# Kernel optimization log

Measured on AMD Instinct MI355X. Metric: run time of the kernel, lower is better.

## Reference

```python
import jax, jax.numpy as jnp
import numpy as np
from jax import lax

NORM = 8.0  # SFA_neuron Norm and Quant max_value
NUM_HEADS = 8

@jax.custom_vjp
def quant(u):
    return jnp.round(jnp.clip(u, 0.0, NORM))

def _quant_fwd(u):
    return quant(u), u

def _quant_bwd(u, g):
    # straight-through: zero grad where input outside [0, NORM]
    return (jnp.where((u >= 0.0) & (u <= NORM), g, 0.0),)

quant.defvjp(_quant_fwd, _quant_bwd)

def sfa(x):
    # x: [T, ...]; recurrent membrane state h carried across timesteps
    def step(h, xt):
        u = h + xt
        s = quant(u)
        return u - s, s / NORM
    _, y = lax.scan(step, jnp.zeros_like(x[0]), x)
    return y

def conv_bn(x, w, scale, bias):
    # 1x1 conv (no bias) + BatchNorm2d (inference, folded to affine)
    # x: [T,B,Cin,H,W], w: [Cout,Cin]
    y = jnp.einsum('oc,tbchw->tbohw', w, x)
    return y * scale[None, None, :, None, None] + bias[None, None, :, None, None]

def setup_inputs() -> dict:
    key = jax.random.key(0)
    ks = jax.random.split(key, 13)
    T, B, C, H, W = 4, 32, 512, 16, 16
    Cv = 4 * C  # lamda_ratio = 4
    f32 = jnp.float32
    d = {}
    d['x'] = jax.random.normal(ks[0], (T, B, C, H, W), f32)
    d['wq'] = jax.random.normal(ks[1], (C, C), f32) * (1.0 / np.sqrt(C))
    d['wk'] = jax.random.normal(ks[2], (C, C), f32) * (1.0 / np.sqrt(C))
    d['wv'] = jax.random.normal(ks[3], (Cv, C), f32) * (1.0 / np.sqrt(C))
    d['wp'] = jax.random.normal(ks[4], (C, Cv), f32) * (1.0 / np.sqrt(Cv))
    d['q_scale'] = 1.0 + 0.1 * jax.random.normal(ks[5], (C,), f32)
    d['q_bias'] = 0.1 * jax.random.normal(ks[6], (C,), f32)
    d['k_scale'] = 1.0 + 0.1 * jax.random.normal(ks[7], (C,), f32)
    d['k_bias'] = 0.1 * jax.random.normal(ks[8], (C,), f32)
    d['v_scale'] = 1.0 + 0.1 * jax.random.normal(ks[9], (Cv,), f32)
    d['v_bias'] = 0.1 * jax.random.normal(ks[10], (Cv,), f32)
    d['p_scale'] = 1.0 + 0.1 * jax.random.normal(ks[11], (C,), f32)
    d['p_bias'] = 0.1 * jax.random.normal(ks[12], (C,), f32)
    return d

def _to_heads(t, h):
    # [T,B,C,H,W] -> [T,B,h,N,C//h]  (channel c -> head c//dh, feat c%dh)
    T_, B_, C_, H_, W_ = t.shape
    return t.reshape(T_, B_, h, C_ // h, H_ * W_).transpose(0, 1, 2, 4, 3)

def reference(x, wq, wk, wv, wp, q_scale, q_bias, k_scale, k_bias, v_scale, v_bias, p_scale, p_bias):
    T, B, C, H, W = x.shape
    N = H * W
    Cv = wv.shape[0]
    scale = (C // NUM_HEADS) ** -0.5

    xs = sfa(x)  # head_spike
    q = sfa(conv_bn(xs, wq, q_scale, q_bias))
    k = sfa(conv_bn(xs, wk, k_scale, k_bias))
    v = sfa(conv_bn(xs, wv, v_scale, v_bias))

    qh = _to_heads(q, NUM_HEADS)  # [T,B,h,N,dh]
    kh = _to_heads(k, NUM_HEADS)
    vh = _to_heads(v, NUM_HEADS)  # [T,B,h,N,dv]

    attn = jnp.einsum('tbhnd,tbhmd->tbhnm', qh, kh)          # [T,B,h,N,N]
    out = jnp.einsum('tbhnm,tbhme->tbhne', attn, vh) * (scale * 2.0)

    out = out.transpose(0, 1, 2, 4, 3).reshape(T, B, Cv, N)  # [T,B,Cv,N]
    out = sfa(out)                                            # attn_spike
    out = out.reshape(T, B, Cv, H, W)
    out = conv_bn(out, wp, p_scale, p_bias)                   # [T,B,C,H,W]
    return out
```

## Files before the change

### kernel.cpp

```cpp
#include <hip/hip_runtime.h>
#include <hip/hip_bf16.h>

#define T_  4
#define B_  32
#define C_  512
#define CV_ 2048
#define N_  256
#define NH_ 8
#define DH_ 64
#define DV_ 256

typedef __bf16 bf16_t;
typedef __bf16 bf16x8 __attribute__((ext_vector_type(8)));
typedef float  f32x4  __attribute__((ext_vector_type(4)));
typedef unsigned char u8x8 __attribute__((ext_vector_type(8)));

#if defined(__has_builtin)
# if __has_builtin(__builtin_amdgcn_global_load_lds)
#  define USE_GLL 1
# endif
#endif

__device__ __forceinline__ f32x4 mfma16(bf16x8 a, bf16x8 b, f32x4 c) {
  return __builtin_amdgcn_mfma_f32_16x16x32_bf16(a, b, c, 0, 0, 0);
}

__device__ __forceinline__ float quant_step(float u) {
  return rintf(fminf(fmaxf(u, 0.0f), 8.0f));
}

__device__ __forceinline__ bf16x8 cvt8(u8x8 v) {
  bf16x8 r;
#pragma unroll
  for (int j = 0; j < 8; ++j) r[j] = (bf16_t)(float)(unsigned int)v[j];
  return r;
}

__device__ __forceinline__ void stage16(const void* g, void* lbase, int lane) {
#ifdef USE_GLL
  __builtin_amdgcn_global_load_lds(
      (const __attribute__((address_space(1))) void*)g,
      (__attribute__((address_space(3))) void*)lbase, 16, 0, 0);
#else
  *(uint4*)((char*)lbase + lane * 16) = *(const uint4*)g;
#endif
}

__global__ __launch_bounds__(256) void k0_split(const float* __restrict__ src,
                                                bf16_t* __restrict__ hi,
                                                bf16_t* __restrict__ lo, int n8) {
  int i = blockIdx.x * 256 + threadIdx.x;
  if (i >= n8) return;
  const float* s = src + (size_t)i * 8;
  bf16x8 h, l;
#pragma unroll
  for (int j = 0; j < 8; ++j) {
    float w = s[j];
    __bf16 hh = (__bf16)w;
    h[j] = hh;
    l[j] = (__bf16)(w - (float)hh);
  }
  *(bf16x8*)(hi + (size_t)i * 8) = h;
  *(bf16x8*)(lo + (size_t)i * 8) = l;
}

__global__ __launch_bounds__(256) void k1_sfa_x(const float* __restrict__ x,
                                                unsigned char* __restrict__ xsT) {
  __shared__ unsigned char tile[64 * 80];
  int bt = blockIdx.x;
  int b  = blockIdx.y;
  int tid = threadIdx.x;
  int c0 = (bt >> 2) * 64, n0 = (bt & 3) * 64;
  int cl = tid >> 2, nc = (tid & 3) * 16;
  int nl = tid >> 2, cj = (tid & 3) * 16;

  float h[16];
#pragma unroll
  for (int j = 0; j < 16; ++j) h[j] = 0.0f;

  for (int t = 0; t < T_; ++t) {
    const float* xp = x + ((size_t)(t * B_ + b) * C_ + c0 + cl) * N_ + n0 + nc;
    f32x4 xv[4];
#pragma unroll
    for (int j = 0; j < 4; ++j) xv[j] = *(const f32x4*)(xp + j * 4);
    if (t) __syncthreads();
#pragma unroll
    for (int j = 0; j < 16; ++j) {
      float u = __fadd_rn(h[j], xv[j >> 2][j & 3]);
      float s = quant_step(u);
      h[j] = __fsub_rn(u, s);
      tile[(nc + j) * 80 + cl] = (unsigned char)s;
    }
    __syncthreads();
    uint4 o = *(const uint4*)&tile[nl * 80 + cj];
    *(uint4*)(xsT + ((size_t)(t * B_ + b) * N_ + n0 + nl) * C_ + c0 + cj) = o;
  }
}

template<bool SWAPQ>
__global__ __launch_bounds__(256, 3) void k2_qkv(
    const unsigned char* __restrict__ xsT,
    const bf16_t* __restrict__ w_hi, const bf16_t* __restrict__ w_lo,
    const float* __restrict__ q_scale, const float* __restrict__ q_bias,
    const float* __restrict__ k_scale, const float* __restrict__ k_bias,
    const float* __restrict__ v_scale, const float* __restrict__ v_bias,
    unsigned char* __restrict__ q_s8, unsigned char* __restrict__ k_s8,
    unsigned char* __restrict__ v_s8, int ct_off) {
  __shared__ __align__(16) unsigned char xs_l[T_][4][1024];
  __shared__ __align__(16) bf16_t whi_l[64 * 64];
  __shared__ __align__(16) bf16_t wlo_l[64 * 64];

  int ct = blockIdx.x + ct_off;
  int ntile = blockIdx.y, b = blockIdx.z;
  int tid = threadIdx.x;
  int w = tid >> 6, lane = tid & 63, quad = lane >> 4, l16 = lane & 15;

  int mode, co_out;
  const float *scp, *bip;
  if (ct < 8)       { mode = 0; co_out = ct * 64;        scp = q_scale; bip = q_bias; }
  else if (ct < 16) { mode = 1; co_out = (ct - 8) * 64;  scp = k_scale; bip = k_bias; }
  else              { mode = 2; co_out = (ct - 16) * 64; scp = v_scale; bip = v_bias; }

  const bf16_t* wrow = w_hi + (size_t)ct * 64 * C_;
  const bf16_t* lrow = w_lo + (size_t)ct * 64 * C_;
  int n0b = ntile * 64;

  int r4 = lane >> 2, m4 = lane & 3;
  int sw4 = (r4 + (r4 >> 2)) & 3;
  int r8 = lane >> 3, m8 = lane & 7;

  f32x4 acc[T_][4];
#pragma unroll
  for (int t = 0; t < T_; ++t)
#pragma unroll
    for (int mt = 0; mt < 4; ++mt) acc[t][mt] = (f32x4){0.f, 0.f, 0.f, 0.f};

  for (int kc = 0; kc < 8; ++kc) {
    int c0 = kc * 64;
    __syncthreads();
#pragma unroll
    for (int t = 0; t < T_; ++t) {
      const unsigned char* g = xsT +
          ((size_t)(t * B_ + b) * N_ + n0b + w * 16 + r4) * C_ + c0 + ((m4 ^ sw4) << 4);
      stage16(g, &xs_l[t][w][0], lane);
    }
#pragma unroll
    for (int j = 0; j < 2; ++j) {
      int r0 = w * 16 + j * 8;
      int row = r0 + r8;
      int col = c0 + ((m8 ^ (row & 7)) << 3);
      stage16(wrow + (size_t)row * C_ + col, (char*)whi_l + r0 * 128, lane);
      stage16(lrow + (size_t)row * C_ + col, (char*)wlo_l + r0 * 128, lane);
    }
    __syncthreads();
#pragma unroll
    for (int ks = 0; ks < 2; ++ks) {
      int kb = ks * 4 + quad;
      int slot = (kb >> 1) ^ ((l16 + (l16 >> 2)) & 3);
      int xoff = l16 * 64 + slot * 16 + (kb & 1) * 8;
      bf16x8 bx[T_];
#pragma unroll
      for (int t = 0; t < T_; ++t)
        bx[t] = cvt8(*(const u8x8*)((const char*)&xs_l[t][w][0] + xoff));
#pragma unroll
      for (int mt = 0; mt < 4; ++mt) {
        int row = mt * 16 + l16;
        int woff = row * 128 + ((kb ^ (row & 7)) << 4);
        bf16x8 ah = *(const bf16x8*)((const char*)whi_l + woff);
        bf16x8 al = *(const bf16x8*)((const char*)wlo_l + woff);
#pragma unroll
        for (int t = 0; t < T_; ++t) {
          if (SWAPQ) {
            acc[t][mt] = mfma16(bx[t], ah, acc[t][mt]);
            acc[t][mt] = mfma16(bx[t], al, acc[t][mt]);
          } else {
            acc[t][mt] = mfma16(ah, bx[t], acc[t][mt]);
            acc[t][mt] = mfma16(al, bx[t], acc[t][mt]);
          }
        }
      }
    }
  }
  if (SWAPQ) {
    float sc[4], bi[4], h[4][4];
#pragma unroll
    for (int mt = 0; mt < 4; ++mt) {
      int c = co_out + mt * 16 + l16;
      sc[mt] = __fmul_rn(q_scale[c], 0.125f);
      bi[mt] = q_bias[c];
#pragma unroll
      for (int r = 0; r < 4; ++r) h[mt][r] = 0.0f;
    }
#pragma unroll
    for (int t = 0; t < T_; ++t)
#pragma unroll
      for (int mt = 0; mt < 4; ++mt)
#pragma unroll
        for (int r = 0; r < 4; ++r) {
          float y = __fmul_rn(acc[t][mt][r], sc[mt]);
          y = __fadd_rn(y, bi[mt]);
          float u = __fadd_rn(h[mt][r], y);
          float s = quant_step(u);
          h[mt][r] = __fsub_rn(u, s);
          int n = n0b + w * 16 + quad * 4 + r;
          int c = co_out + mt * 16 + l16;
          q_s8[((size_t)(t * B_ + b) * N_ + n) * C_ + c] = (unsigned char)s;
        }
  } else {
    float sc[4][4], bi[4][4], h[4][4];
#pragma unroll
    for (int mt = 0; mt < 4; ++mt)
#pragma unroll
      for (int r = 0; r < 4; ++r) {
        int c = co_out + mt * 16 + quad * 4 + r;
        sc[mt][r] = __fmul_rn(scp[c], 0.125f);
        bi[mt][r] = bip[c];
        h[mt][r] = 0.0f;
      }
#pragma unroll
    for (int t = 0; t < T_; ++t)
#pragma unroll
      for (int mt = 0; mt < 4; ++mt)
#pragma unroll
        for (int r = 0; r < 4; ++r) {
          float y = __fmul_rn(acc[t][mt][r], sc[mt][r]);
          y = __fadd_rn(y, bi[mt][r]);
          float u = __fadd_rn(h[mt][r], y);
          float s = quant_step(u);
          h[mt][r] = __fsub_rn(u, s);
          int n = n0b + w * 16 + l16;
          int c = co_out + mt * 16 + quad * 4 + r;
          unsigned char sp = (unsigned char)s;
          if (mode == 1) k_s8[((size_t)(t * B_ + b) * C_ + c) * N_ + n] = sp;
          else           v_s8[((size_t)(t * B_ + b) * CV_ + c) * N_ + n] = sp;
        }
  }
}

__global__ __launch_bounds__(256) void k3_attn(
    const unsigned char* __restrict__ q_s8, const unsigned char* __restrict__ k_s8,
    const unsigned char* __restrict__ v_s8, unsigned char* __restrict__ a_s8) {
  __shared__ float kvbuf[64 * 68];
  int et = blockIdx.x, hh = blockIdx.y, b = blockIdx.z;
  int tid = threadIdx.x;
  int w = tid >> 6, lane = tid & 63, quad = lane >> 4, l16 = lane & 15;
  int e0 = et * 64;

  f32x4 Aacc[4][4];
#pragma unroll
  for (int mt = 0; mt < 4; ++mt)
#pragma unroll
    for (int nt = 0; nt < 4; ++nt) Aacc[mt][nt] = (f32x4){0.f, 0.f, 0.f, 0.f};

  for (int t = 0; t < T_; ++t) {
    size_t tb = (size_t)(t * B_ + b);
    f32x4 kva[4];
#pragma unroll
    for (int et2 = 0; et2 < 4; ++et2) kva[et2] = (f32x4){0.f, 0.f, 0.f, 0.f};
    const unsigned char* krow  = k_s8 + ((size_t)tb * C_ + hh * DH_ + w * 16 + l16) * N_;
    const unsigned char* vbase = v_s8 + ((size_t)tb * CV_ + hh * DV_ + e0) * N_;
    for (int kc = 0; kc < 8; ++kc) {
      int koff = kc * 32 + quad * 8;
      bf16x8 a = cvt8(*(const u8x8*)(krow + koff));
#pragma unroll
      for (int et2 = 0; et2 < 4; ++et2) {
        bf16x8 bb = cvt8(*(const u8x8*)(vbase + (size_t)(et2 * 16 + l16) * N_ + koff));
        kva[et2] = mfma16(a, bb, kva[et2]);
      }
    }
    __syncthreads();
#pragma unroll
    for (int et2 = 0; et2 < 4; ++et2)
#pragma unroll
      for (int r = 0; r < 4; ++r)
        kvbuf[(w * 16 + quad * 4 + r) * 68 + et2 * 16 + l16] = kva[et2][r];
    __syncthreads();

    const unsigned char* qrow = q_s8 + ((size_t)tb * N_ + w * 64) * C_ + hh * DH_;
    for (int kc2 = 0; kc2 < 2; ++kc2) {
      int kbase = kc2 * 32 + quad * 8;
      bf16x8 bq[4];
#pragma unroll
      for (int nt = 0; nt < 4; ++nt)
        bq[nt] = cvt8(*(const u8x8*)(qrow + (size_t)(nt * 16 + l16) * C_ + kbase));
#pragma unroll
      for (int mt = 0; mt < 4; ++mt) {
        bf16x8 ahi, alo;
#pragma unroll
        for (int j = 0; j < 8; ++j) {
          float v = kvbuf[(kbase + j) * 68 + mt * 16 + l16] * 0.015625f;
          __bf16 hi = (__bf16)v;
          ahi[j] = hi;
          alo[j] = (__bf16)(v - (float)hi);
        }
#pragma unroll
        for (int nt = 0; nt < 4; ++nt) {
          Aacc[mt][nt] = mfma16(ahi, bq[nt], Aacc[mt][nt]);
          Aacc[mt][nt] = mfma16(alo, bq[nt], Aacc[mt][nt]);
        }
      }
    }
#pragma unroll
    for (int mt = 0; mt < 4; ++mt)
#pragma unroll
      for (int nt = 0; nt < 4; ++nt)
#pragma unroll
        for (int r = 0; r < 4; ++r) {
          float u = Aacc[mt][nt][r] * 0.03125f;
          float s = quant_step(u);
          int cv = hh * DV_ + e0 + mt * 16 + quad * 4 + r;
          int n  = w * 64 + nt * 16 + l16;
          a_s8[(tb * N_ + n) * CV_ + cv] = (unsigned char)s;
          Aacc[mt][nt][r] = __fsub_rn(Aacc[mt][nt][r], 32.0f * s);
        }
  }
}

__global__ __launch_bounds__(256, 3) void k4_pconv(
    const unsigned char* __restrict__ a_s8,
    const bf16_t* __restrict__ wp_hi, const bf16_t* __restrict__ wp_lo,
    const float* __restrict__ p_scale, const float* __restrict__ p_bias,
    float* __restrict__ out) {
  __shared__ __align__(16) unsigned char as_l[4][4][1024];
  __shared__ __align__(16) bf16_t whi_l[64 * 64];
  __shared__ __align__(16) bf16_t wlo_l[64 * 64];

  int ct = blockIdx.x, ntile = blockIdx.y, tbq = blockIdx.z;
  int tid = threadIdx.x;
  int w = tid >> 6, lane = tid & 63, quad = lane >> 4, l16 = lane & 15;
  int co0 = ct * 64, n0b = ntile * 64;

  int r4 = lane >> 2, m4 = lane & 3;
  int sw4 = (r4 + (r4 >> 2)) & 3;
  int r8 = lane >> 3, m8 = lane & 7;

  const bf16_t* wrow = wp_hi + (size_t)co0 * CV_;
  const bf16_t* lrow = wp_lo + (size_t)co0 * CV_;

  f32x4 acc[4][4];
#pragma unroll
  for (int i = 0; i < 4; ++i)
#pragma unroll
    for (int mt = 0; mt < 4; ++mt) acc[i][mt] = (f32x4){0.f, 0.f, 0.f, 0.f};

  for (int kc = 0; kc < 32; ++kc) {
    int c0 = kc * 64;
    __syncthreads();
#pragma unroll
    for (int tbi = 0; tbi < 4; ++tbi) {
      const unsigned char* g = a_s8 +
          ((size_t)(tbq * 4 + tbi) * N_ + n0b + w * 16 + r4) * CV_ + c0 + ((m4 ^ sw4) << 4);
      stage16(g, &as_l[tbi][w][0], lane);
    }
#pragma unroll
    for (int j = 0; j < 2; ++j) {
      int r0 = w * 16 + j * 8;
      int row = r0 + r8;
      int col = c0 + ((m8 ^ (row & 7)) << 3);
      stage16(wrow + (size_t)row * CV_ + col, (char*)whi_l + r0 * 128, lane);
      stage16(lrow + (size_t)row * CV_ + col, (char*)wlo_l + r0 * 128, lane);
    }
    __syncthreads();
#pragma unroll
    for (int ks = 0; ks < 2; ++ks) {
      int kb = ks * 4 + quad;
      int slot = (kb >> 1) ^ ((l16 + (l16 >> 2)) & 3);
      int xoff = l16 * 64 + slot * 16 + (kb & 1) * 8;
      bf16x8 bx[4];
#pragma unroll
      for (int tbi = 0; tbi < 4; ++tbi)
        bx[tbi] = cvt8(*(const u8x8*)((const char*)&as_l[tbi][w][0] + xoff));
#pragma unroll
      for (int mt = 0; mt < 4; ++mt) {
        int row = mt * 16 + l16;
        int woff = row * 128 + ((kb ^ (row & 7)) << 4);
        bf16x8 ah = *(const bf16x8*)((const char*)whi_l + woff);
        bf16x8 al = *(const bf16x8*)((const char*)wlo_l + woff);
#pragma unroll
        for (int tbi = 0; tbi < 4; ++tbi) {
          acc[tbi][mt] = mfma16(ah, bx[tbi], acc[tbi][mt]);
          acc[tbi][mt] = mfma16(al, bx[tbi], acc[tbi][mt]);
        }
      }
    }
  }
#pragma unroll
  for (int mt = 0; mt < 4; ++mt)
#pragma unroll
    for (int r = 0; r < 4; ++r) {
      int c = co0 + mt * 16 + quad * 4 + r;
      float scv = __fmul_rn(p_scale[c], 0.125f);
      float biv = p_bias[c];
#pragma unroll
      for (int tbi = 0; tbi < 4; ++tbi) {
        float y = __fmul_rn(acc[tbi][mt][r], scv);
        y = __fadd_rn(y, biv);
        int n = n0b + w * 16 + l16;
        out[((size_t)(tbq * 4 + tbi) * C_ + c) * N_ + n] = y;
      }
    }
}

extern "C" void kernel_launch(void* const* d_in, const int* in_sizes, int n_in,
                              void* d_out, int out_size, void* d_ws, size_t ws_size,
                              hipStream_t stream) {
  const float* x       = (const float*)d_in[0];
  const float* wq      = (const float*)d_in[1];
  const float* wk      = (const float*)d_in[2];
  const float* wv      = (const float*)d_in[3];
  const float* wp      = (const float*)d_in[4];
  const float* q_scale = (const float*)d_in[5];
  const float* q_bias  = (const float*)d_in[6];
  const float* k_scale = (const float*)d_in[7];
  const float* k_bias  = (const float*)d_in[8];
  const float* v_scale = (const float*)d_in[9];
  const float* v_bias  = (const float*)d_in[10];
  const float* p_scale = (const float*)d_in[11];
  const float* p_bias  = (const float*)d_in[12];

  const size_t MB = 1024 * 1024;
  if (ws_size < 160 * MB) return;
  char* ws = (char*)d_ws;
  unsigned char* xsT    = (unsigned char*)(ws);
  unsigned char* a_s8   = (unsigned char*)(ws);
  bf16_t*        wqkv_h = (bf16_t*)(ws + 32 * MB);
  bf16_t*        wqkv_l = (bf16_t*)(ws + 35 * MB);
  unsigned char* q_s8   = (unsigned char*)(ws + 64 * MB);
  bf16_t*        wp_h   = (bf16_t*)(ws + 64 * MB);
  bf16_t*        wp_l   = (bf16_t*)(ws + 66 * MB);
  unsigned char* k_s8   = (unsigned char*)(ws + 80 * MB);
  unsigned char* v_s8   = (unsigned char*)(ws + 96 * MB);

  k0_split<<<128, 256, 0, stream>>>(wq, wqkv_h, wqkv_l, 32768);
  k0_split<<<128, 256, 0, stream>>>(wk, wqkv_h + 262144, wqkv_l + 262144, 32768);
  k0_split<<<512, 256, 0, stream>>>(wv, wqkv_h + 524288, wqkv_l + 524288, 131072);

  k1_sfa_x<<<dim3(32, B_), 256, 0, stream>>>(x, xsT);
  k2_qkv<true><<<dim3(8, 4, B_), 256, 0, stream>>>(
      xsT, wqkv_h, wqkv_l, q_scale, q_bias, k_scale, k_bias,
      v_scale, v_bias, q_s8, k_s8, v_s8, 0);
  k2_qkv<false><<<dim3(40, 4, B_), 256, 0, stream>>>(
      xsT, wqkv_h, wqkv_l, q_scale, q_bias, k_scale, k_bias,
      v_scale, v_bias, q_s8, k_s8, v_s8, 8);
  k3_attn<<<dim3(4, NH_, B_), 256, 0, stream>>>(q_s8, k_s8, v_s8, a_s8);
  k0_split<<<512, 256, 0, stream>>>(wp, wp_h, wp_l, 131072);
  k4_pconv<<<dim3(8, 4, B_), 256, 0, stream>>>(a_s8, wp_h, wp_l,
                                               p_scale, p_bias, (float*)d_out);
}
```

Baseline: 586.5 us.

## Double-buffer LDS staging in QKV and projection conv kernels

Converts the k2_qkv and k4_pconv main loops to a double-buffered LDS pipeline. The next K-chunk is prefetched into the alternate buffer while the current one is consumed by MFMAs, and one barrier per iteration replaces two. s_setprio is raised around the MFMA section. The larger shared-memory footprint comes with a launch_bounds occupancy hint lowered from 3 to 2 blocks per CU, trading occupancy for latency hiding.

```diff
diff --git a/kernel.cpp b/kernel.cpp
--- a/kernel.cpp
+++ b/kernel.cpp
@@ -98,7 +98,7 @@
 }
 
 template<bool SWAPQ>
-__global__ __launch_bounds__(256, 3) void k2_qkv(
+__global__ __launch_bounds__(256, 2) void k2_qkv(
     const unsigned char* __restrict__ xsT,
     const bf16_t* __restrict__ w_hi, const bf16_t* __restrict__ w_lo,
     const float* __restrict__ q_scale, const float* __restrict__ q_bias,
@@ -106,9 +106,9 @@
     const float* __restrict__ v_scale, const float* __restrict__ v_bias,
     unsigned char* __restrict__ q_s8, unsigned char* __restrict__ k_s8,
     unsigned char* __restrict__ v_s8, int ct_off) {
-  __shared__ __align__(16) unsigned char xs_l[T_][4][1024];
-  __shared__ __align__(16) bf16_t whi_l[64 * 64];
-  __shared__ __align__(16) bf16_t wlo_l[64 * 64];
+  __shared__ __align__(16) unsigned char xs_l[2][T_][4][1024];
+  __shared__ __align__(16) bf16_t whi_l[2][64 * 64];
+  __shared__ __align__(16) bf16_t wlo_l[2][64 * 64];
 
   int ct = blockIdx.x + ct_off;
   int ntile = blockIdx.y, b = blockIdx.z;
@@ -135,24 +135,31 @@
 #pragma unroll
     for (int mt = 0; mt < 4; ++mt) acc[t][mt] = (f32x4){0.f, 0.f, 0.f, 0.f};
 
-  for (int kc = 0; kc < 8; ++kc) {
+  auto STAGE = [&](int kc, int pb) {
     int c0 = kc * 64;
-    __syncthreads();
 #pragma unroll
     for (int t = 0; t < T_; ++t) {
       const unsigned char* g = xsT +
           ((size_t)(t * B_ + b) * N_ + n0b + w * 16 + r4) * C_ + c0 + ((m4 ^ sw4) << 4);
-      stage16(g, &xs_l[t][w][0], lane);
+      stage16(g, &xs_l[pb][t][w][0], lane);
     }
 #pragma unroll
     for (int j = 0; j < 2; ++j) {
       int r0 = w * 16 + j * 8;
       int row = r0 + r8;
       int col = c0 + ((m8 ^ (row & 7)) << 3);
-      stage16(wrow + (size_t)row * C_ + col, (char*)whi_l + r0 * 128, lane);
-      stage16(lrow + (size_t)row * C_ + col, (char*)wlo_l + r0 * 128, lane);
-    }
-    __syncthreads();
+      stage16(wrow + (size_t)row * C_ + col, (char*)&whi_l[pb][0] + r0 * 128, lane);
+      stage16(lrow + (size_t)row * C_ + col, (char*)&wlo_l[pb][0] + r0 * 128, lane);
+    }
+  };
+
+  STAGE(0, 0);
+  __syncthreads();
+
+  for (int kc = 0; kc < 8; ++kc) {
+    int pb = kc & 1;
+    if (kc < 7) STAGE(kc + 1, pb ^ 1);
+    __builtin_amdgcn_s_setprio(1);
 #pragma unroll
     for (int ks = 0; ks < 2; ++ks) {
       int kb = ks * 4 + quad;
@@ -161,13 +168,13 @@
       bf16x8 bx[T_];
 #pragma unroll
       for (int t = 0; t < T_; ++t)
-        bx[t] = cvt8(*(const u8x8*)((const char*)&xs_l[t][w][0] + xoff));
+        bx[t] = cvt8(*(const u8x8*)((const char*)&xs_l[pb][t][w][0] + xoff));
 #pragma unroll
       for (int mt = 0; mt < 4; ++mt) {
         int row = mt * 16 + l16;
         int woff = row * 128 + ((kb ^ (row & 7)) << 4);
-        bf16x8 ah = *(const bf16x8*)((const char*)whi_l + woff);
-        bf16x8 al = *(const bf16x8*)((const char*)wlo_l + woff);
+        bf16x8 ah = *(const bf16x8*)((const char*)&whi_l[pb][0] + woff);
+        bf16x8 al = *(const bf16x8*)((const char*)&wlo_l[pb][0] + woff);
 #pragma unroll
         for (int t = 0; t < T_; ++t) {
           if (SWAPQ) {
@@ -180,6 +187,8 @@
         }
       }
     }
+    __builtin_amdgcn_s_setprio(0);
+    __syncthreads();
   }
   if (SWAPQ) {
     float sc[4], bi[4], h[4][4];
@@ -316,14 +325,14 @@
   }
 }
 
-__global__ __launch_bounds__(256, 3) void k4_pconv(
+__global__ __launch_bounds__(256, 2) void k4_pconv(
     const unsigned char* __restrict__ a_s8,
     const bf16_t* __restrict__ wp_hi, const bf16_t* __restrict__ wp_lo,
     const float* __restrict__ p_scale, const float* __restrict__ p_bias,
     float* __restrict__ out) {
-  __shared__ __align__(16) unsigned char as_l[4][4][1024];
-  __shared__ __align__(16) bf16_t whi_l[64 * 64];
-  __shared__ __align__(16) bf16_t wlo_l[64 * 64];
+  __shared__ __align__(16) unsigned char as_l[2][4][4][1024];
+  __shared__ __align__(16) bf16_t whi_l[2][64 * 64];
+  __shared__ __align__(16) bf16_t wlo_l[2][64 * 64];
 
   int ct = blockIdx.x, ntile = blockIdx.y, tbq = blockIdx.z;
   int tid = threadIdx.x;
@@ -343,24 +352,31 @@
 #pragma unroll
     for (int mt = 0; mt < 4; ++mt) acc[i][mt] = (f32x4){0.f, 0.f, 0.f, 0.f};
 
-  for (int kc = 0; kc < 32; ++kc) {
+  auto STAGE = [&](int kc, int pb) {
     int c0 = kc * 64;
-    __syncthreads();
 #pragma unroll
     for (int tbi = 0; tbi < 4; ++tbi) {
       const unsigned char* g = a_s8 +
           ((size_t)(tbq * 4 + tbi) * N_ + n0b + w * 16 + r4) * CV_ + c0 + ((m4 ^ sw4) << 4);
-      stage16(g, &as_l[tbi][w][0], lane);
+      stage16(g, &as_l[pb][tbi][w][0], lane);
     }
 #pragma unroll
     for (int j = 0; j < 2; ++j) {
       int r0 = w * 16 + j * 8;
       int row = r0 + r8;
       int col = c0 + ((m8 ^ (row & 7)) << 3);
-      stage16(wrow + (size_t)row * CV_ + col, (char*)whi_l + r0 * 128, lane);
-      stage16(lrow + (size_t)row * CV_ + col, (char*)wlo_l + r0 * 128, lane);
-    }
-    __syncthreads();
+      stage16(wrow + (size_t)row * CV_ + col, (char*)&whi_l[pb][0] + r0 * 128, lane);
+      stage16(lrow + (size_t)row * CV_ + col, (char*)&wlo_l[pb][0] + r0 * 128, lane);
+    }
+  };
+
+  STAGE(0, 0);
+  __syncthreads();
+
+  for (int kc = 0; kc < 32; ++kc) {
+    int pb = kc & 1;
+    if (kc < 31) STAGE(kc + 1, pb ^ 1);
+    __builtin_amdgcn_s_setprio(1);
 #pragma unroll
     for (int ks = 0; ks < 2; ++ks) {
       int kb = ks * 4 + quad;
@@ -369,13 +385,13 @@
       bf16x8 bx[4];
 #pragma unroll
       for (int tbi = 0; tbi < 4; ++tbi)
-        bx[tbi] = cvt8(*(const u8x8*)((const char*)&as_l[tbi][w][0] + xoff));
+        bx[tbi] = cvt8(*(const u8x8*)((const char*)&as_l[pb][tbi][w][0] + xoff));
 #pragma unroll
       for (int mt = 0; mt < 4; ++mt) {
         int row = mt * 16 + l16;
         int woff = row * 128 + ((kb ^ (row & 7)) << 4);
-        bf16x8 ah = *(const bf16x8*)((const char*)whi_l + woff);
-        bf16x8 al = *(const bf16x8*)((const char*)wlo_l + woff);
+        bf16x8 ah = *(const bf16x8*)((const char*)&whi_l[pb][0] + woff);
+        bf16x8 al = *(const bf16x8*)((const char*)&wlo_l[pb][0] + woff);
 #pragma unroll
         for (int tbi = 0; tbi < 4; ++tbi) {
           acc[tbi][mt] = mfma16(ah, bx[tbi], acc[tbi][mt]);
@@ -383,6 +399,8 @@
         }
       }
     }
+    __builtin_amdgcn_s_setprio(0);
+    __syncthreads();
   }
 #pragma unroll
   for (int mt = 0; mt < 4; ++mt)
```

After: 602.9 us. +2.8%, slower.
